# Kernel tuning notes

Hardware: AMD Instinct MI355X
Metric: run time of the kernel (lower is better)

## Reference

```python
import jax, jax.numpy as jnp
import numpy as np

STOCH, DETER, HIDDEN, A, EMBED = 30, 200, 200, 6, 1024
T, B = 64, 512
MIN_STD = 0.1
LN_EPS = 1e-3


def _ln(x, s, b):
    m = jnp.mean(x, -1, keepdims=True)
    v = jnp.mean((x - m) ** 2, -1, keepdims=True)
    return (x - m) * jax.lax.rsqrt(v + LN_EPS) * s + b


def _stats(x):
    mean, std = jnp.split(x, 2, -1)
    return mean, jax.nn.softplus(std) + MIN_STD


def setup_inputs() -> dict:
    key = jax.random.key(0)
    ks = jax.random.split(key, 12)
    w = lambda k, shape, s=0.05: jax.random.normal(k, shape, jnp.float32) * s
    return dict(
        embed=w(ks[0], (T, B, EMBED), 1.0),
        action=w(ks[1], (T, B, A), 1.0),
        is_first=jax.random.randint(ks[2], (T, B), 0, 2).astype(jnp.float32),
        noise_prior=w(ks[3], (T, B, STOCH), 1.0),
        noise_post=w(ks[4], (T, B, STOCH), 1.0),
        w_inp=w(ks[5], (STOCH + A, HIDDEN)),
        ln_inp_s=jnp.ones((HIDDEN,)), ln_inp_b=jnp.zeros((HIDDEN,)),
        w_gru=w(ks[6], (HIDDEN + DETER, 3 * DETER)),
        w_imgout=w(ks[7], (DETER, HIDDEN)),
        ln_img_s=jnp.ones((HIDDEN,)), ln_img_b=jnp.zeros((HIDDEN,)),
        w_obsout=w(ks[8], (DETER + EMBED, HIDDEN)),
        ln_obs_s=jnp.ones((HIDDEN,)), ln_obs_b=jnp.zeros((HIDDEN,)),
        w_ims=w(ks[9], (HIDDEN, 2 * STOCH)), b_ims=jnp.zeros((2 * STOCH,)),
        w_obs=w(ks[10], (HIDDEN, 2 * STOCH)), b_obs=jnp.zeros((2 * STOCH,)),
        w_init=w(ks[11], (1, DETER), 0.1),
    )


def reference(embed, action, is_first, noise_prior, noise_post,
              w_inp, ln_inp_s, ln_inp_b, w_gru, w_imgout, ln_img_s, ln_img_b,
              w_obsout, ln_obs_s, ln_obs_b, w_ims, b_ims, w_obs, b_obs, w_init):
    # learned initial state: deter0 = tanh(W), stoch0 = mode (mean) of img stats
    deter0 = jnp.tanh(w_init) * jnp.ones((B, 1), embed.dtype)          # [B, DETER]
    h0 = jax.nn.silu(_ln(deter0 @ w_imgout, ln_img_s, ln_img_b))
    stoch0, _ = _stats(h0 @ w_ims + b_ims)                              # [B, STOCH]

    def step(carry, xs):
        stoch, deter = carry
        a_t, e_t, f_t, nzp, nzq = xs
        # action magnitude clip with stop-gradient scale
        a = a_t * jax.lax.stop_gradient(1.0 / jnp.maximum(jnp.abs(a_t), 1.0))
        f = f_t[:, None]
        a = a * (1.0 - f)
        stoch = stoch * (1.0 - f) + stoch0 * f
        deter = deter * (1.0 - f) + deter0 * f
        # img_step (prior): inp layers -> GRU cell -> img_out -> stats
        x = jax.nn.silu(_ln(jnp.concatenate([stoch, a], -1) @ w_inp, ln_inp_s, ln_inp_b))
        parts = jnp.concatenate([x, deter], -1) @ w_gru                 # [B, 3*DETER]
        r, c, u = jnp.split(parts, 3, -1)
        r = jax.nn.sigmoid(r)
        c = jnp.tanh(r * c)
        u = jax.nn.sigmoid(u - 1.0)                                     # update_bias = -1
        deter = u * c + (1.0 - u) * deter
        hp = jax.nn.silu(_ln(deter @ w_imgout, ln_img_s, ln_img_b))
        pm, ps = _stats(hp @ w_ims + b_ims)
        prior_stoch = pm + ps * nzp                                     # rsample
        # obs_step (posterior, temp_post=True): concat(deter, embed)
        ho = jax.nn.silu(_ln(jnp.concatenate([deter, e_t], -1) @ w_obsout, ln_obs_s, ln_obs_b))
        qm, qs = _stats(ho @ w_obs + b_obs)
        post_stoch = qm + qs * nzq
        out_t = jnp.concatenate([qm, qs, post_stoch, pm, ps, prior_stoch, deter], -1)
        return (post_stoch, deter), out_t

    _, out = jax.lax.scan(step, (stoch0, deter0),
                          (action, embed, is_first, noise_prior, noise_post))
    return out  # [T, B, 6*STOCH + DETER] = post(mean,std,stoch), prior(mean,std,stoch), deter
```

## Files before the change

kernel.cpp:

```cpp
#include <hip/hip_runtime.h>
#include <math.h>

#define T_STEPS 64
#define BATCH   512

typedef short s16x8 __attribute__((ext_vector_type(8)));
typedef float f32x4 __attribute__((ext_vector_type(4)));

#define MFMA(a,b,c) __builtin_amdgcn_mfma_f32_16x16x32_bf16((a),(b),(c),0,0,0)

__device__ __forceinline__ short f2bf(float x){
    union { float f; unsigned u; } v; v.f = x;
    unsigned r = v.u + 0x7FFFu + ((v.u >> 16) & 1u);
    return (short)(r >> 16);
}
__device__ __forceinline__ float bf2f(short s){
    union { unsigned u; float f; } v; v.u = ((unsigned)(unsigned short)s) << 16;
    return v.f;
}
__device__ __forceinline__ float frcp(float x){ return __builtin_amdgcn_rcpf(x); }
__device__ __forceinline__ float fsig(float x){ return frcp(1.f + __expf(-x)); }
__device__ __forceinline__ float ftanh(float x){ return 1.f - 2.f*frcp(1.f + __expf(2.f*x)); }
__device__ __forceinline__ float sp(float x){ return (x>20.f)? x : __logf(1.f + __expf(x)); }

__device__ __forceinline__ void barx(){
    asm volatile("s_waitcnt lgkmcnt(0)" ::: "memory");
    __builtin_amdgcn_s_barrier();
    asm volatile("" ::: "memory");
}

#define FR_GRU   0
#define FR_INP   494
#define FR_OBSD  520
#define FR_OBSE  611
#define FR_OBS   1027
#define FR_IMG   1055
#define FR_IMS   1146
#define FR_TOT   1174

#define WS_STOCH0 1202176
#define WS_DETER0 1202304
#define WS_E      1203200

__global__ void pack_kernel(const float* w_inp, const float* w_gru, const float* w_imgout,
                            const float* w_obsout, const float* w_ims, const float* w_obs,
                            short* pk){
    int f = blockIdx.x, l = threadIdx.x;
    const float* W; int K, N, ld, KT, k0, rel;
    if      (f < FR_INP ){ W=w_gru;    K=400; N=600; ld=600; KT=13; k0=0;   rel=f; }
    else if (f < FR_OBSD){ W=w_inp;    K=36;  N=200; ld=200; KT=2;  k0=0;   rel=f-FR_INP; }
    else if (f < FR_OBSE){ W=w_obsout; K=200; N=200; ld=200; KT=7;  k0=0;   rel=f-FR_OBSD; }
    else if (f < FR_OBS ){ W=w_obsout; K=1024;N=200; ld=200; KT=32; k0=200; rel=f-FR_OBSE; }
    else if (f < FR_IMG ){ W=w_obs;    K=200; N=60;  ld=60;  KT=7;  k0=0;   rel=f-FR_OBS; }
    else if (f < FR_IMS ){ W=w_imgout; K=200; N=200; ld=200; KT=7;  k0=0;   rel=f-FR_IMG; }
    else                 { W=w_ims;    K=200; N=60;  ld=60;  KT=7;  k0=0;   rel=f-FR_IMS; }
    int nt = rel / KT, kt = rel % KT;
    int col = nt*16 + (l & 15);
    int kb  = kt*32 + (l >> 4)*8;
    s16x8 v;
    #pragma unroll
    for (int e = 0; e < 8; e++){
        int k = kb + e;
        float x = (k < K && col < N) ? W[(size_t)(k + k0)*ld + col] : 0.f;
        v[e] = f2bf(x);
    }
    *(((s16x8*)pk) + (size_t)f*64 + l) = v;
}

__global__ void init_kernel(const float* w_init, const float* w_imgout,
                            const float* ln_img_s, const float* ln_img_b,
                            const float* w_ims, const float* b_ims,
                            float* stoch0, float* deter0){
    __shared__ float d0[200], h0[200], redA[64], redB[64], mv[2];
    int t = threadIdx.x;
    if (t < 200) d0[t] = tanhf(w_init[t]);
    __syncthreads();
    if (t < 200){ float a = 0.f; for (int k = 0; k < 200; k++) a += d0[k]*w_imgout[k*200 + t]; h0[t] = a; }
    __syncthreads();
    if (t < 64){ float s = 0.f, s2 = 0.f;
        for (int j = t; j < 200; j += 64){ float v = h0[j]; s += v; s2 += v*v; }
        redA[t] = s; redB[t] = s2; }
    __syncthreads();
    if (t == 0){ float s = 0.f, s2 = 0.f;
        for (int i = 0; i < 64; i++){ s += redA[i]; s2 += redB[i]; }
        float m = s/200.f, var = s2/200.f - m*m;
        mv[0] = m; mv[1] = rsqrtf(var + 1e-3f); }
    __syncthreads();
    if (t < 200){ float v = (h0[t]-mv[0])*mv[1]*ln_img_s[t] + ln_img_b[t];
        h0[t] = v/(1.f+expf(-v)); }
    __syncthreads();
    if (t < 200) deter0[t] = d0[t];
    if (t < 30){ float a = 0.f; for (int j = 0; j < 200; j++) a += h0[j]*w_ims[j*60 + t];
        stoch0[t] = a + b_ims[t]; }
}

__global__ __launch_bounds__(256) void embed_gemm(const float* embed, const short* pk, short* E){
    int tid = threadIdx.x; int w = tid >> 6, l = tid & 63;
    int row0 = blockIdx.x*128 + w*32;
    const float* A0 = embed + (size_t)(row0 + (l & 15))*1024 + (l >> 4)*8;
    const float* A1 = A0 + (size_t)16*1024;
    const s16x8* B = ((const s16x8*)pk) + (size_t)FR_OBSE*64 + l;
    f32x4 acc0[13], acc1[13];
    #pragma unroll
    for (int n = 0; n < 13; n++){ acc0[n] = (f32x4){0.f,0.f,0.f,0.f}; acc1[n] = (f32x4){0.f,0.f,0.f,0.f}; }
    for (int kt = 0; kt < 32; kt++){
        float4 x0 = *(const float4*)(A0 + kt*32), x1 = *(const float4*)(A0 + kt*32 + 4);
        float4 y0 = *(const float4*)(A1 + kt*32), y1 = *(const float4*)(A1 + kt*32 + 4);
        s16x8 af0, af1;
        af0[0]=f2bf(x0.x); af0[1]=f2bf(x0.y); af0[2]=f2bf(x0.z); af0[3]=f2bf(x0.w);
        af0[4]=f2bf(x1.x); af0[5]=f2bf(x1.y); af0[6]=f2bf(x1.z); af0[7]=f2bf(x1.w);
        af1[0]=f2bf(y0.x); af1[1]=f2bf(y0.y); af1[2]=f2bf(y0.z); af1[3]=f2bf(y0.w);
        af1[4]=f2bf(y1.x); af1[5]=f2bf(y1.y); af1[6]=f2bf(y1.z); af1[7]=f2bf(y1.w);
        #pragma unroll
        for (int n = 0; n < 13; n++){
            s16x8 bf = B[(n*32 + kt)*64];
            acc0[n] = MFMA(af0, bf, acc0[n]);
            acc1[n] = MFMA(af1, bf, acc1[n]);
        }
    }
    int rr = (l >> 4)*4, cc = l & 15;
    #pragma unroll
    for (int n = 0; n < 13; n++){
        int col = n*16 + cc;
        if (col < 200){
            #pragma unroll
            for (int r = 0; r < 4; r++){
                E[(size_t)(row0 + rr + r)*200 + col]        = f2bf(acc0[n][r]);
                E[(size_t)(row0 + 16 + rr + r)*200 + col]   = f2bf(acc1[n][r]);
            }
        }
    }
}

#define AB_STRIDE 424
#define XP_STRIDE 210
#define PB_STRIDE 612
#define QP_STRIDE 68
#define A36_STRIDE 72
#define HO_STRIDE 224

__global__ __launch_bounds__(512) void scan_kernel(
    const float* action, const float* is_first, const float* noise_post,
    const float* ln_inp_s, const float* ln_inp_b,
    const float* ln_obs_s, const float* ln_obs_b,
    const float* b_obs,
    const short* pk, const short* E, const float* stoch0g, const float* deter0g,
    float* out)
{
    __shared__ short Abuf[16*AB_STRIDE];
    __shared__ __align__(16) char Uraw[19584];
    __shared__ short A36hob[16*HO_STRIDE];
    __shared__ float Sbuf[8*30];
    __shared__ short WI[26*512];
    __shared__ short WD[91*512];

    float* Uf  = (float*)Uraw;
    short* Pbs = (short*)Uraw;

    int tid = threadIdx.x;
    int w = tid >> 6, l = tid & 63;
    int row = tid >> 6;
    int s = tid & 63;
    int r0 = blockIdx.x*8;
    const int rr = (l >> 4)*4, cc = l & 15;
    const s16x8* PK = (const s16x8*)pk;

    for (int f = w; f < 26; f += 8)
        *(s16x8*)&WI[f*512 + l*8] = PK[(size_t)(FR_INP + f)*64 + l];
    for (int f = w; f < 91; f += 8)
        *(s16x8*)&WD[f*512 + l*8] = PK[(size_t)(FR_OBSD + f)*64 + l];

    float dreg[4];
    #pragma unroll
    for (int i = 0; i < 4; i++){ int j = s + 64*i; dreg[i] = (j < 200) ? deter0g[j] : 0.f; }
    if (s < 30 && row == 0){}
    if (tid < 8*30){ int rw = tid/30, j = tid%30; Sbuf[rw*30 + j] = stoch0g[j]; }

    for (int idx = tid; idx < 8*AB_STRIDE; idx += 512) Abuf[(8 + idx/AB_STRIDE)*AB_STRIDE + idx%AB_STRIDE] = 0;
    for (int idx = tid; idx < 8*24; idx += 512) Abuf[(idx/24)*AB_STRIDE + 400 + idx%24] = 0;
    for (int idx = tid; idx < 8*200; idx += 512) Abuf[(idx/200)*AB_STRIDE + idx%200] = 0;
    for (int idx = tid; idx < 3008; idx += 512) A36hob[576 + idx] = 0;
    #pragma unroll
    for (int i = 0; i < 4; i++){ int j = s + 64*i; if (j < 200) Abuf[row*AB_STRIDE + 200 + j] = f2bf(dreg[i]); }

    float lisr[4], libr[4], losr[4], lobr[4];
    #pragma unroll
    for (int i = 0; i < 4; i++){ int j = s + 64*i; bool ok = j < 200;
        lisr[i] = ok ? ln_inp_s[j] : 0.f;  libr[i] = ok ? ln_inp_b[j] : 0.f;
        losr[i] = ok ? ln_obs_s[j] : 0.f;  lobr[i] = ok ? ln_obs_b[j] : 0.f;
    }
    float bo0 = 0.f, bo1 = 0.f;
    if (tid < 240){ int j = tid % 30; bo0 = b_obs[j]; bo1 = b_obs[30 + j]; }

    barx();

    for (int t = 0; t < T_STEPS; t++){
        float f = is_first[(size_t)t*BATCH + r0 + row];
        #pragma unroll
        for (int i = 0; i < 4; i++){ int j = s + 64*i; if (j < 200){
            float d = dreg[i]*(1.f - f) + deter0g[j]*f;
            dreg[i] = d;
            Abuf[row*AB_STRIDE + 200 + j] = f2bf(d);
        }}
        {
            int j = s;
            float v = 0.f;
            if (j < 30) v = Sbuf[row*30 + j]*(1.f - f) + stoch0g[j]*f;
            else if (j < 36){
                float a = action[(size_t)((size_t)t*BATCH + r0 + row)*6 + (j - 30)];
                a = a * frcp(fmaxf(fabsf(a), 1.f));
                v = a*(1.f - f);
            }
            A36hob[row*A36_STRIDE + j] = f2bf(v);
        }
        if (tid < 568) A36hob[576 + tid] = 0;
        s16x8 Ech;
        if (tid < 200){
            int er = tid/25, eq = tid%25;
            Ech = *(((const s16x8*)(E + (size_t)((size_t)t*BATCH + r0 + er)*200)) + eq);
        }
        float nz = 0.f;
        if (tid < 240){
            int rw = tid/30, j = tid%30;
            nz = noise_post[(size_t)((size_t)t*BATCH + r0 + rw)*30 + j];
        }
        barx();

        {
            s16x8 a0 = *(s16x8*)&A36hob[(l & 15)*A36_STRIDE + (l >> 4)*8];
            s16x8 a1 = *(s16x8*)&A36hob[(l & 15)*A36_STRIDE + 32 + (l >> 4)*8];
            for (int nt = w; nt < 13; nt += 8){
                f32x4 acc = (f32x4){0.f,0.f,0.f,0.f};
                acc = MFMA(a0, *(const s16x8*)&WI[(nt*2+0)*512 + l*8], acc);
                acc = MFMA(a1, *(const s16x8*)&WI[(nt*2+1)*512 + l*8], acc);
                #pragma unroll
                for (int r = 0; r < 4; r++) Uf[(rr + r)*XP_STRIDE + nt*16 + cc] = acc[r];
            }
        }
        barx();

        {
            float sum = 0.f, sq = 0.f, vals[4];
            #pragma unroll
            for (int i = 0; i < 4; i++){ int j = s + 64*i;
                float v = (j < 200) ? Uf[row*XP_STRIDE + j] : 0.f;
                vals[i] = v; sum += v; sq += v*v; }
            #pragma unroll
            for (int m = 32; m >= 1; m >>= 1){ sum += __shfl_xor(sum, m); sq += __shfl_xor(sq, m); }
            float mean = sum/200.f, var = sq/200.f - mean*mean, rstd = rsqrtf(var + 1e-3f);
            #pragma unroll
            for (int i = 0; i < 4; i++){ int j = s + 64*i; if (j < 200){
                float v = (vals[i] - mean)*rstd*lisr[i] + libr[i];
                Abuf[row*AB_STRIDE + j] = f2bf(v*fsig(v));
            }}
        }
        barx();

        {
            s16x8 af[13];
            #pragma unroll
            for (int kt = 0; kt < 13; kt++)
                af[kt] = *(s16x8*)&Abuf[(l & 15)*AB_STRIDE + kt*32 + (l >> 4)*8];
            for (int nt = w; nt < 38; nt += 8){
                f32x4 acc = (f32x4){0.f,0.f,0.f,0.f};
                const s16x8* B = PK + (size_t)(FR_GRU + nt*13)*64 + l;
                #pragma unroll
                for (int kt = 0; kt < 13; kt++) acc = MFMA(af[kt], B[kt*64], acc);
                #pragma unroll
                for (int r = 0; r < 4; r++) Pbs[(rr + r)*PB_STRIDE + nt*16 + cc] = f2bf(acc[r]);
            }
        }
        barx();

        {
            float* outp = out + (size_t)((size_t)t*BATCH + r0 + row)*380;
            #pragma unroll
            for (int i = 0; i < 4; i++){ int j = s + 64*i; if (j < 200){
                float rv = bf2f(Pbs[row*PB_STRIDE + j]);
                float cv = bf2f(Pbs[row*PB_STRIDE + 200 + j]);
                float uv = bf2f(Pbs[row*PB_STRIDE + 400 + j]);
                float rg = fsig(rv);
                float cg = ftanh(rg*cv);
                float ug = fsig(uv - 1.f);
                float d  = ug*cg + (1.f - ug)*dreg[i];
                dreg[i] = d;
                Abuf[row*AB_STRIDE + 200 + j] = f2bf(d);
                outp[180 + j] = d;
            }}
        }
        barx();

        {
            s16x8 ad[7];
            #pragma unroll
            for (int kt = 0; kt < 7; kt++)
                ad[kt] = *(s16x8*)&Abuf[(l & 15)*AB_STRIDE + 200 + kt*32 + (l >> 4)*8];
            for (int nt = w; nt < 13; nt += 8){
                f32x4 a0={0.f,0.f,0.f,0.f}, a1={0.f,0.f,0.f,0.f};
                a0 = MFMA(ad[0], *(const s16x8*)&WD[(nt*7+0)*512 + l*8], a0);
                a1 = MFMA(ad[1], *(const s16x8*)&WD[(nt*7+1)*512 + l*8], a1);
                a0 = MFMA(ad[2], *(const s16x8*)&WD[(nt*7+2)*512 + l*8], a0);
                a1 = MFMA(ad[3], *(const s16x8*)&WD[(nt*7+3)*512 + l*8], a1);
                a0 = MFMA(ad[4], *(const s16x8*)&WD[(nt*7+4)*512 + l*8], a0);
                a1 = MFMA(ad[5], *(const s16x8*)&WD[(nt*7+5)*512 + l*8], a1);
                a0 = MFMA(ad[6], *(const s16x8*)&WD[(nt*7+6)*512 + l*8], a0);
                #pragma unroll
                for (int r = 0; r < 4; r++) Uf[(rr + r)*XP_STRIDE + nt*16 + cc] = a0[r]+a1[r];
            }
        }
        barx();

        if (tid < 200){
            int er = tid/25, eq = tid%25;
            #pragma unroll
            for (int e = 0; e < 8; e++) Uf[er*XP_STRIDE + eq*8 + e] += bf2f(Ech[e]);
        }
        barx();

        {
            float sum = 0.f, sq = 0.f, vals[4];
            #pragma unroll
            for (int i = 0; i < 4; i++){ int j = s + 64*i;
                float v = (j < 200) ? Uf[row*XP_STRIDE + j] : 0.f;
                vals[i] = v; sum += v; sq += v*v; }
            #pragma unroll
            for (int m = 32; m >= 1; m >>= 1){ sum += __shfl_xor(sum, m); sq += __shfl_xor(sq, m); }
            float mean = sum/200.f, var = sq/200.f - mean*mean, rstd = rsqrtf(var + 1e-3f);
            #pragma unroll
            for (int i = 0; i < 4; i++){ int j = s + 64*i;
                if (j < 224){
                    short hv = 0;
                    if (j < 200){
                        float v = (vals[i] - mean)*rstd*losr[i] + lobr[i];
                        hv = f2bf(v*fsig(v));
                    }
                    A36hob[row*HO_STRIDE + j] = hv;
                }
            }
        }
        barx();

        if (w < 4){
            s16x8 ah[7];
            #pragma unroll
            for (int kt = 0; kt < 7; kt++)
                ah[kt] = *(s16x8*)&A36hob[(l & 15)*HO_STRIDE + kt*32 + (l >> 4)*8];
            f32x4 a0={0.f,0.f,0.f,0.f}, a1={0.f,0.f,0.f,0.f};
            const s16x8* B = PK + (size_t)(FR_OBS + w*7)*64 + l;
            a0=MFMA(ah[0],B[0*64],a0); a1=MFMA(ah[1],B[1*64],a1);
            a0=MFMA(ah[2],B[2*64],a0); a1=MFMA(ah[3],B[3*64],a1);
            a0=MFMA(ah[4],B[4*64],a0); a1=MFMA(ah[5],B[5*64],a1);
            a0=MFMA(ah[6],B[6*64],a0);
            #pragma unroll
            for (int r = 0; r < 4; r++) Uf[(rr + r)*QP_STRIDE + w*16 + cc] = a0[r]+a1[r];
        }
        barx();

        if (tid < 240){
            int rw = tid/30, j = tid%30;
            float qm = Uf[rw*QP_STRIDE + j] + bo0;
            float x  = Uf[rw*QP_STRIDE + 30 + j] + bo1;
            float qs = sp(x) + 0.1f;
            float post = qm + qs*nz;
            float* outp = out + (size_t)((size_t)t*BATCH + r0 + rw)*380;
            outp[j] = qm; outp[30 + j] = qs; outp[60 + j] = post;
            Sbuf[rw*30 + j] = post;
        }
        barx();
    }
}

__global__ __launch_bounds__(64) void prior_kernel(const float* noise_prior, const float* b_ims,
                                                   const float* ln_img_s, const float* ln_img_b,
                                                   const short* pk, float* out){
    __shared__ short Ab[16*232];
    __shared__ float U[16*212];
    __shared__ short hob[16*224];
    __shared__ float qp[16*68];
    int l = threadIdx.x;
    int g0 = blockIdx.x*16;

    for (int idx = l; idx < 16*232; idx += 64){
        int rr = idx/232, c = idx%232;
        short v = 0;
        if (c < 200) v = f2bf(out[(size_t)(g0 + rr)*380 + 180 + c]);
        Ab[idx] = v;
    }
    __syncthreads();
    {
        s16x8 af[7];
        #pragma unroll
        for (int kt = 0; kt < 7; kt++)
            af[kt] = *(s16x8*)&Ab[(l & 15)*232 + kt*32 + (l >> 4)*8];
        for (int nt = 0; nt < 13; nt++){
            f32x4 acc = (f32x4){0.f,0.f,0.f,0.f};
            const s16x8* B = ((const s16x8*)pk) + (size_t)(FR_IMG + nt*7)*64 + l;
            #pragma unroll
            for (int kt = 0; kt < 7; kt++) acc = MFMA(af[kt], B[kt*64], acc);
            int rr = (l >> 4)*4, cc = l & 15;
            #pragma unroll
            for (int r = 0; r < 4; r++) U[(rr + r)*212 + nt*16 + cc] = acc[r];
        }
    }
    __syncthreads();
    {
        int rw = l >> 2, s4 = l & 3;
        float sum = 0.f, sq = 0.f, vals[50];
        #pragma unroll
        for (int i = 0; i < 50; i++){ int j = s4 + 4*i; float v = U[rw*212 + j];
            vals[i] = v; sum += v; sq += v*v; }
        sum += __shfl_xor(sum, 1); sq += __shfl_xor(sq, 1);
        sum += __shfl_xor(sum, 2); sq += __shfl_xor(sq, 2);
        float mean = sum/200.f, var = sq/200.f - mean*mean, rstd = rsqrtf(var + 1e-3f);
        #pragma unroll
        for (int i = 0; i < 50; i++){ int j = s4 + 4*i;
            float v = (vals[i] - mean)*rstd*ln_img_s[j] + ln_img_b[j];
            hob[rw*224 + j] = f2bf(v*fsig(v));
        }
    }
    for (int idx = l; idx < 16*24; idx += 64){ int rr = idx/24; hob[rr*224 + 200 + idx%24] = 0; }
    __syncthreads();
    for (int nt = 0; nt < 4; nt++){
        s16x8 af[7];
        #pragma unroll
        for (int kt = 0; kt < 7; kt++)
            af[kt] = *(s16x8*)&hob[(l & 15)*224 + kt*32 + (l >> 4)*8];
        f32x4 acc = (f32x4){0.f,0.f,0.f,0.f};
        const s16x8* B = ((const s16x8*)pk) + (size_t)(FR_IMS + nt*7)*64 + l;
        #pragma unroll
        for (int kt = 0; kt < 7; kt++) acc = MFMA(af[kt], B[kt*64], acc);
        int rr = (l >> 4)*4, cc = l & 15;
        #pragma unroll
        for (int r = 0; r < 4; r++) qp[(rr + r)*68 + nt*16 + cc] = acc[r];
    }
    __syncthreads();
    for (int idx = l; idx < 480; idx += 64){
        int rw = idx/30, j = idx%30;
        float pm = qp[rw*68 + j] + b_ims[j];
        float x  = qp[rw*68 + 30 + j] + b_ims[30 + j];
        float ps = sp(x) + 0.1f;
        float nz = noise_prior[(size_t)(g0 + rw)*30 + j];
        float prior = pm + ps*nz;
        float* op = out + (size_t)(g0 + rw)*380;
        op[90 + j] = pm; op[120 + j] = ps; op[150 + j] = prior;
    }
}

extern "C" void kernel_launch(void* const* d_in, const int* in_sizes, int n_in,
                              void* d_out, int out_size, void* d_ws, size_t ws_size,
                              hipStream_t stream){
    const float* embed    = (const float*)d_in[0];
    const float* action   = (const float*)d_in[1];
    const float* is_first = (const float*)d_in[2];
    const float* nzp      = (const float*)d_in[3];
    const float* nzq      = (const float*)d_in[4];
    const float* w_inp    = (const float*)d_in[5];
    const float* ln_inp_s = (const float*)d_in[6];
    const float* ln_inp_b = (const float*)d_in[7];
    const float* w_gru    = (const float*)d_in[8];
    const float* w_imgout = (const float*)d_in[9];
    const float* ln_img_s = (const float*)d_in[10];
    const float* ln_img_b = (const float*)d_in[11];
    const float* w_obsout = (const float*)d_in[12];
    const float* ln_obs_s = (const float*)d_in[13];
    const float* ln_obs_b = (const float*)d_in[14];
    const float* w_ims    = (const float*)d_in[15];
    const float* b_ims    = (const float*)d_in[16];
    const float* w_obs    = (const float*)d_in[17];
    const float* b_obs    = (const float*)d_in[18];
    const float* w_init   = (const float*)d_in[19];

    char*  ws    = (char*)d_ws;
    short* pk    = (short*)ws;
    float* stoch0 = (float*)(ws + WS_STOCH0);
    float* deter0 = (float*)(ws + WS_DETER0);
    short* E      = (short*)(ws + WS_E);
    float* out    = (float*)d_out;

    hipLaunchKernelGGL(pack_kernel, dim3(FR_TOT), dim3(64), 0, stream,
                       w_inp, w_gru, w_imgout, w_obsout, w_ims, w_obs, pk);
    hipLaunchKernelGGL(init_kernel, dim3(1), dim3(256), 0, stream,
                       w_init, w_imgout, ln_img_s, ln_img_b, w_ims, b_ims, stoch0, deter0);
    hipLaunchKernelGGL(embed_gemm, dim3(256), dim3(256), 0, stream, embed, pk, E);
    hipLaunchKernelGGL(scan_kernel, dim3(64), dim3(512), 0, stream,
                       action, is_first, nzq, ln_inp_s, ln_inp_b, ln_obs_s, ln_obs_b, b_obs,
                       pk, E, stoch0, deter0, out);
    hipLaunchKernelGGL(prior_kernel, dim3(2048), dim3(64), 0, stream, nzp, b_ims, ln_img_s, ln_img_b, pk, out);
}
```

Measured before the change: 818.0 us.

## Stream GRU and obs weights through LDS with async global_load_lds double-buffering

Replaces the resident LDS copies of the input and obs-deter weights with a per-wave staging area filled by asynchronous global_load_lds. The GRU weight fragments, previously read straight from global memory inside the MFMA loop, are now prefetched one iteration ahead, with vmcnt waits splitting each tile into two halves. Obs-deter weights are prefetched during the GRU elementwise phase so the load overlaps that work. The input projection now reads its weights from global instead of LDS. The trade-off is weights re-fetched from L2 every timestep and carefully hand-counted waitcnts that must match the issue order exactly.

```diff
diff --git a/kernel.cpp b/kernel.cpp
--- a/kernel.cpp
+++ b/kernel.cpp
@@ -27,6 +27,14 @@
     asm volatile("s_waitcnt lgkmcnt(0)" ::: "memory");
     __builtin_amdgcn_s_barrier();
     asm volatile("" ::: "memory");
+}
+#define WAITV(n) asm volatile("s_waitcnt vmcnt(" #n ")" ::: "memory")
+#define LGKM0    asm volatile("s_waitcnt lgkmcnt(0)" ::: "memory")
+
+typedef const __attribute__((address_space(1))) void* gas_t;
+typedef __attribute__((address_space(3))) void* las_t;
+__device__ __forceinline__ void gld16(const void* g, void* l){
+    __builtin_amdgcn_global_load_lds((gas_t)g, (las_t)l, 16, 0, 0);
 }
 
 #define FR_GRU   0
@@ -151,8 +159,7 @@
     __shared__ __align__(16) char Uraw[19584];
     __shared__ short A36hob[16*HO_STRIDE];
     __shared__ float Sbuf[8*30];
-    __shared__ short WI[26*512];
-    __shared__ short WD[91*512];
+    __shared__ __align__(16) short SG[8*14*512];
 
     float* Uf  = (float*)Uraw;
     short* Pbs = (short*)Uraw;
@@ -164,16 +171,51 @@
     int r0 = blockIdx.x*8;
     const int rr = (l >> 4)*4, cc = l & 15;
     const s16x8* PK = (const s16x8*)pk;
-
-    for (int f = w; f < 26; f += 8)
-        *(s16x8*)&WI[f*512 + l*8] = PK[(size_t)(FR_INP + f)*64 + l];
-    for (int f = w; f < 91; f += 8)
-        *(s16x8*)&WD[f*512 + l*8] = PK[(size_t)(FR_OBSD + f)*64 + l];
+    const char* pkb = (const char*)pk;
+
+#define SGR(slot) (*(const s16x8*)&SG[w*7168 + (slot)*512 + l*8])
+#define ISSUE_LO(ITV) do{ size_t fb = (size_t)(FR_GRU + (w + (ITV)*8)*13)*1024; \
+    _Pragma("unroll") for (int f_ = 0; f_ < 7; f_++) \
+        gld16(pkb + fb + (size_t)f_*1024 + l*16, &SG[w*7168 + f_*512]); }while(0)
+#define ISSUE_HI(ITV) do{ size_t fb = (size_t)(FR_GRU + (w + (ITV)*8)*13 + 7)*1024; \
+    _Pragma("unroll") for (int f_ = 0; f_ < 6; f_++) \
+        gld16(pkb + fb + (size_t)f_*1024 + l*16, &SG[w*7168 + (7+f_)*512]); }while(0)
+
+#define MM2_MID(ITV) do{ \
+    f32x4 p0={0.f,0.f,0.f,0.f}, p1={0.f,0.f,0.f,0.f}; \
+    WAITV(6); \
+    p0=MFMA(af[0],SGR(0),p0); p1=MFMA(af[1],SGR(1),p1); \
+    p0=MFMA(af[2],SGR(2),p0); p1=MFMA(af[3],SGR(3),p1); \
+    p0=MFMA(af[4],SGR(4),p0); p1=MFMA(af[5],SGR(5),p1); \
+    p0=MFMA(af[6],SGR(6),p0); \
+    LGKM0; ISSUE_LO(ITV+1); \
+    WAITV(7); \
+    p1=MFMA(af[7],SGR(7),p1);  p0=MFMA(af[8],SGR(8),p0); \
+    p1=MFMA(af[9],SGR(9),p1);  p0=MFMA(af[10],SGR(10),p0); \
+    p1=MFMA(af[11],SGR(11),p1); p0=MFMA(af[12],SGR(12),p0); \
+    LGKM0; ISSUE_HI(ITV+1); \
+    { int nt_ = w + (ITV)*8; \
+      _Pragma("unroll") for (int r=0;r<4;r++) Pbs[(rr+r)*PB_STRIDE + nt_*16 + cc] = f2bf(p0[r]+p1[r]); } \
+}while(0)
+
+#define MM2_LAST(ITV) do{ \
+    f32x4 p0={0.f,0.f,0.f,0.f}, p1={0.f,0.f,0.f,0.f}; \
+    WAITV(6); \
+    p0=MFMA(af[0],SGR(0),p0); p1=MFMA(af[1],SGR(1),p1); \
+    p0=MFMA(af[2],SGR(2),p0); p1=MFMA(af[3],SGR(3),p1); \
+    p0=MFMA(af[4],SGR(4),p0); p1=MFMA(af[5],SGR(5),p1); \
+    p0=MFMA(af[6],SGR(6),p0); \
+    WAITV(0); \
+    p1=MFMA(af[7],SGR(7),p1);  p0=MFMA(af[8],SGR(8),p0); \
+    p1=MFMA(af[9],SGR(9),p1);  p0=MFMA(af[10],SGR(10),p0); \
+    p1=MFMA(af[11],SGR(11),p1); p0=MFMA(af[12],SGR(12),p0); \
+    { int nt_ = w + (ITV)*8; \
+      _Pragma("unroll") for (int r=0;r<4;r++) Pbs[(rr+r)*PB_STRIDE + nt_*16 + cc] = f2bf(p0[r]+p1[r]); } \
+}while(0)
 
     float dreg[4];
     #pragma unroll
     for (int i = 0; i < 4; i++){ int j = s + 64*i; dreg[i] = (j < 200) ? deter0g[j] : 0.f; }
-    if (s < 30 && row == 0){}
     if (tid < 8*30){ int rw = tid/30, j = tid%30; Sbuf[rw*30 + j] = stoch0g[j]; }
 
     for (int idx = tid; idx < 8*AB_STRIDE; idx += 512) Abuf[(8 + idx/AB_STRIDE)*AB_STRIDE + idx%AB_STRIDE] = 0;
@@ -224,6 +266,8 @@
             int rw = tid/30, j = tid%30;
             nz = noise_post[(size_t)((size_t)t*BATCH + r0 + rw)*30 + j];
         }
+        ISSUE_LO(0);
+        ISSUE_HI(0);
         barx();
 
         {
@@ -231,8 +275,9 @@
             s16x8 a1 = *(s16x8*)&A36hob[(l & 15)*A36_STRIDE + 32 + (l >> 4)*8];
             for (int nt = w; nt < 13; nt += 8){
                 f32x4 acc = (f32x4){0.f,0.f,0.f,0.f};
-                acc = MFMA(a0, *(const s16x8*)&WI[(nt*2+0)*512 + l*8], acc);
-                acc = MFMA(a1, *(const s16x8*)&WI[(nt*2+1)*512 + l*8], acc);
+                const s16x8* B = PK + (size_t)(FR_INP + nt*2)*64 + l;
+                acc = MFMA(a0, B[0],  acc);
+                acc = MFMA(a1, B[64], acc);
                 #pragma unroll
                 for (int r = 0; r < 4; r++) Uf[(rr + r)*XP_STRIDE + nt*16 + cc] = acc[r];
             }
@@ -261,17 +306,26 @@
             #pragma unroll
             for (int kt = 0; kt < 13; kt++)
                 af[kt] = *(s16x8*)&Abuf[(l & 15)*AB_STRIDE + kt*32 + (l >> 4)*8];
-            for (int nt = w; nt < 38; nt += 8){
-                f32x4 acc = (f32x4){0.f,0.f,0.f,0.f};
-                const s16x8* B = PK + (size_t)(FR_GRU + nt*13)*64 + l;
+            if (w < 6){
+                MM2_MID(0); MM2_MID(1); MM2_MID(2); MM2_MID(3); MM2_LAST(4);
+            } else {
+                MM2_MID(0); MM2_MID(1); MM2_MID(2); MM2_LAST(3);
+            }
+        }
+        barx();
+
+        {
+            size_t fb = (size_t)(FR_OBSD + w*7)*1024;
+            #pragma unroll
+            for (int f_ = 0; f_ < 7; f_++)
+                gld16(pkb + fb + (size_t)f_*1024 + l*16, &SG[w*7168 + f_*512]);
+            if (w < 5){
+                size_t fb2 = (size_t)(FR_OBSD + (8+w)*7)*1024;
                 #pragma unroll
-                for (int kt = 0; kt < 13; kt++) acc = MFMA(af[kt], B[kt*64], acc);
-                #pragma unroll
-                for (int r = 0; r < 4; r++) Pbs[(rr + r)*PB_STRIDE + nt*16 + cc] = f2bf(acc[r]);
-            }
-        }
-        barx();
-
+                for (int f_ = 0; f_ < 7; f_++)
+                    gld16(pkb + fb2 + (size_t)f_*1024 + l*16, &SG[w*7168 + (7+f_)*512]);
+            }
+        }
         {
             float* outp = out + (size_t)((size_t)t*BATCH + r0 + row)*380;
             #pragma unroll
@@ -291,19 +345,27 @@
         barx();
 
         {
+            WAITV(0);
             s16x8 ad[7];
             #pragma unroll
             for (int kt = 0; kt < 7; kt++)
                 ad[kt] = *(s16x8*)&Abuf[(l & 15)*AB_STRIDE + 200 + kt*32 + (l >> 4)*8];
-            for (int nt = w; nt < 13; nt += 8){
+            {
                 f32x4 a0={0.f,0.f,0.f,0.f}, a1={0.f,0.f,0.f,0.f};
-                a0 = MFMA(ad[0], *(const s16x8*)&WD[(nt*7+0)*512 + l*8], a0);
-                a1 = MFMA(ad[1], *(const s16x8*)&WD[(nt*7+1)*512 + l*8], a1);
-                a0 = MFMA(ad[2], *(const s16x8*)&WD[(nt*7+2)*512 + l*8], a0);
-                a1 = MFMA(ad[3], *(const s16x8*)&WD[(nt*7+3)*512 + l*8], a1);
-                a0 = MFMA(ad[4], *(const s16x8*)&WD[(nt*7+4)*512 + l*8], a0);
-                a1 = MFMA(ad[5], *(const s16x8*)&WD[(nt*7+5)*512 + l*8], a1);
-                a0 = MFMA(ad[6], *(const s16x8*)&WD[(nt*7+6)*512 + l*8], a0);
+                a0=MFMA(ad[0],SGR(0),a0); a1=MFMA(ad[1],SGR(1),a1);
+                a0=MFMA(ad[2],SGR(2),a0); a1=MFMA(ad[3],SGR(3),a1);
+                a0=MFMA(ad[4],SGR(4),a0); a1=MFMA(ad[5],SGR(5),a1);
+                a0=MFMA(ad[6],SGR(6),a0);
+                #pragma unroll
+                for (int r = 0; r < 4; r++) Uf[(rr + r)*XP_STRIDE + w*16 + cc] = a0[r]+a1[r];
+            }
+            if (w < 5){
+                int nt = 8 + w;
+                f32x4 a0={0.f,0.f,0.f,0.f}, a1={0.f,0.f,0.f,0.f};
+                a0=MFMA(ad[0],SGR(7),a0);  a1=MFMA(ad[1],SGR(8),a1);
+                a0=MFMA(ad[2],SGR(9),a0);  a1=MFMA(ad[3],SGR(10),a1);
+                a0=MFMA(ad[4],SGR(11),a0); a1=MFMA(ad[5],SGR(12),a1);
+                a0=MFMA(ad[6],SGR(13),a0);
                 #pragma unroll
                 for (int r = 0; r < 4; r++) Uf[(rr + r)*XP_STRIDE + nt*16 + cc] = a0[r]+a1[r];
             }
```

Result: slower. 1.242 ms (+51.8%).
